# Kernel optimization log

Hardware: AMD Instinct MI355X
Metric: run time of the kernel (lower is better)

The kernel has to match this reference:

```python
import jax, jax.numpy as jnp
import numpy as np

K = 3
S = 1
C_IN = 64
C_OUT = 128

def setup_inputs() -> dict:
    key = jax.random.key(0)
    k1, k2, k3 = jax.random.split(key, 3)
    x = jax.random.normal(k1, (16, C_IN, 256, 256), dtype=jnp.float32)
    weight = jax.random.normal(k2, (C_OUT, C_IN, K, K), dtype=jnp.float32)
    bias = jax.random.normal(k3, (C_OUT,), dtype=jnp.float32)
    return {"x": x, "weight": weight, "bias": bias}

def reference(x, weight, bias):
    # SAME-style padding of k//2 on each side, stride S, output h//S x w//S
    pad = K // 2
    out = jax.lax.conv_general_dilated(
        x, weight,
        window_strides=(S, S),
        padding=[(pad, pad), (pad, pad)],
        dimension_numbers=("NCHW", "OIHW", "NCHW"),
    )
    return out + bias[None, :, None, None]
```

## Files before the change

kernel.cpp:

```cpp
#include <hip/hip_runtime.h>


typedef _Float16 half8_t __attribute__((ext_vector_type(8)));
typedef float floatx4 __attribute__((ext_vector_type(4)));

#define HH 256
#define WW 256
#define CIN 64
#define COUT 128
#define NB 16

#define XP_RSTRIDE   16512
#define XP_NSTRIDE   4260096
#define XP_RSTRIDE_B 33024
#define ROW_LDS      8448
#define TILE_BYTES   50688

__device__ inline void gload_lds16(const void* g, void* l) {
    __builtin_amdgcn_global_load_lds(
        (const __attribute__((address_space(1))) unsigned int*)g,
        (__attribute__((address_space(3))) unsigned int*)l, 16, 0, 0);
}

__global__ void Conv2d_wprep_kernel(const float* __restrict__ w, _Float16* __restrict__ w_t) {
    int idx = blockIdx.x * 256 + threadIdx.x;
    if (idx >= 9 * 8 * 128 * 8) return;
    const int j = idx & 7, cout = (idx >> 3) & 127, s = (idx >> 10) & 7, t = idx >> 13;
    w_t[idx] = (_Float16)w[(cout * 64 + s * 8 + j) * 9 + t];
}

__global__ void Conv2d_xpad_zero_kernel(_Float16* __restrict__ xp) {
    const int idx = blockIdx.x * 256 + threadIdx.x;
    const int n = blockIdx.y;
    if (idx >= 8224) return;
    size_t off;
    if (idx < 2064)      off = (size_t)idx * 8;
    else if (idx < 4128) off = (size_t)257 * XP_RSTRIDE + (size_t)(idx - 2064) * 8;
    else if (idx < 6176) { const int t = idx - 4128;
        off = (size_t)(1 + (t >> 3)) * XP_RSTRIDE + (size_t)(t & 7) * 8; }
    else { const int t = idx - 6176;
        off = (size_t)(1 + (t >> 3)) * XP_RSTRIDE + 257 * 64 + (size_t)(t & 7) * 8; }
    int4 z = {0, 0, 0, 0};
    *(int4*)(xp + (size_t)n * XP_NSTRIDE + off) = z;
}

__global__ __launch_bounds__(256) void Conv2d_xprep_kernel(const float* __restrict__ x,
                                                           _Float16* __restrict__ xp) {
    const int tid = threadIdx.x;
    const int u = tid & 7, colq = tid >> 3;
    const int n = blockIdx.z, h = blockIdx.y;
    const int col0 = blockIdx.x * 128 + colq * 4;

    float4 in[8];
#pragma unroll
    for (int j = 0; j < 8; ++j)
        in[j] = *(const float4*)(x + ((size_t)((n * 64 + u * 8 + j) * 256 + h) * 256) + col0);

    _Float16* dst = xp + (size_t)n * XP_NSTRIDE + (size_t)(h + 1) * XP_RSTRIDE +
                    (size_t)(col0 + 1) * 64 + u * 8;
#pragma unroll
    for (int i = 0; i < 4; ++i) {
        half8_t hv;
#pragma unroll
        for (int j = 0; j < 8; ++j) hv[j] = (_Float16)((const float*)&in[j])[i];
        *(half8_t*)(dst + (size_t)i * 64) = hv;
    }
}

__global__ __launch_bounds__(512, 2) void Conv2dManual_77695958385099_kernel(
    const _Float16* __restrict__ xp, const _Float16* __restrict__ w_t,
    const float* __restrict__ bias, float* __restrict__ out) {
    __shared__ __align__(16) unsigned char xs[2 * TILE_BYTES];
    __shared__ __align__(16) float esc[8][1088];
    const int tid = threadIdx.x;
    const int l = tid & 63, wvid = tid >> 6;
    const int g = l >> 4, ln = l & 15;
    const int ow0 = blockIdx.x * 64;
    const int band = blockIdx.y;
    const int n = blockIdx.z;

    const char* wl = (const char*)w_t + g * 2048 + (wvid * 16 + ln) * 16;
    half8_t A[2][9];
#pragma unroll
    for (int h = 0; h < 2; ++h)
#pragma unroll
        for (int tp = 0; tp < 9; ++tp)
            A[h][tp] = *(const half8_t*)(wl + h * 8192 + tp * 16384);

    const float bv = bias[wvid * 16 + ln];

    int F[4][3][2];
#pragma unroll
    for (int cgf = 0; cgf < 4; ++cgf)
#pragma unroll
        for (int kx = 0; kx < 3; ++kx)
#pragma unroll
            for (int h = 0; h < 2; ++h) {
                const int c = cgf * 16 + kx + ln;
                F[cgf][kx][h] = c * 128 + (((4 * h + g) ^ (c & 7)) << 4);
            }

    const char* xbase = (const char*)xp + (size_t)n * XP_NSTRIDE * 2 + (size_t)ow0 * 128;

#define STAGE(BUFSEL, IT)                                                              \
    {                                                                                  \
        const char* gt = xbase + (size_t)(band * 64 + (IT) * 4) * XP_RSTRIDE_B;        \
        const unsigned lb = (BUFSEL) * TILE_BYTES;                                     \
        _Pragma("unroll")                                                              \
        for (int p = 0; p < 6; ++p) {                                                  \
            const int u = p * 512 + tid;                                               \
            int row = (p * 512) / 528;                                                 \
            if (u >= (row + 1) * 528) row++;                                           \
            const int rem = u - row * 528;                                             \
            const int c = rem >> 3, s = rem & 7;                                       \
            gload_lds16(gt + (size_t)row * XP_RSTRIDE_B + c * 128 +                    \
                            (((s ^ (c & 7))) << 4),                                    \
                        xs + lb + ((unsigned)(p * 512 + (tid & ~63)) << 4));           \
        }                                                                              \
        if (tid < 96) {                                                                \
            const int rem = 432 + tid;                                                 \
            const int c = rem >> 3, s = rem & 7;                                       \
            const int4 v = *(const int4*)(gt + (size_t)5 * XP_RSTRIDE_B + c * 128 +    \
                                          ((s ^ (c & 7)) << 4));                       \
            *(int4*)(xs + lb + (unsigned)(3072 + tid) * 16) = v;                       \
        }                                                                              \
    }

    STAGE(0, 0);
    asm volatile("s_waitcnt vmcnt(0) lgkmcnt(0)" ::: "memory");
    __builtin_amdgcn_s_barrier();
    __builtin_amdgcn_sched_barrier(0);

    int cur = 0;
#pragma unroll 1
    for (int it = 0; it < 16; ++it) {
        if (it < 15) STAGE(cur ^ 1, it + 1);

        floatx4 acc[4][4];
#pragma unroll
        for (int rr = 0; rr < 4; ++rr)
#pragma unroll
            for (int cgf = 0; cgf < 4; ++cgf) acc[rr][cgf] = (floatx4){bv, bv, bv, bv};

        const unsigned char* bb = xs + cur * TILE_BYTES;
#pragma unroll
        for (int kx = 0; kx < 3; ++kx)
#pragma unroll
            for (int h = 0; h < 2; ++h)
#pragma unroll
                for (int cgf = 0; cgf < 4; ++cgf) {
                    const unsigned char* bp = bb + F[cgf][kx][h];
                    half8_t bt[6];
#pragma unroll
                    for (int t = 0; t < 6; ++t)
                        bt[t] = *(const half8_t*)(bp + t * ROW_LDS);
#pragma unroll
                    for (int ky = 0; ky < 3; ++ky) {
                        const half8_t af = A[h][ky * 3 + kx];
#pragma unroll
                        for (int rr = 0; rr < 4; ++rr)
                            acc[rr][cgf] = __builtin_amdgcn_mfma_f32_16x16x32_f16(
                                bt[rr + ky], af, acc[rr][cgf], 0, 0, 0);
                    }
                }

        float* scr = &esc[wvid][0];
        const int orow0 = band * 64 + it * 4;
        float* obase = out + ((size_t)(n * 128 + wvid * 16)) * 65536 +
                       (size_t)orow0 * 256 + ow0;
#pragma unroll
        for (int rr = 0; rr < 4; ++rr) {
#pragma unroll
            for (int cgf = 0; cgf < 4; ++cgf)
                *(floatx4*)(scr + ln * 68 + cgf * 16 + g * 4) = acc[rr][cgf];
#pragma unroll
            for (int q = 0; q < 4; ++q) {
                const int co = q * 4 + g;
                const floatx4 v = *(const floatx4*)(scr + co * 68 + ln * 4);
                __builtin_nontemporal_store(
                    v, (floatx4*)(obase + (size_t)co * 65536 + rr * 256 + ln * 4));
            }
        }

        if (it < 15) {
            asm volatile("s_waitcnt vmcnt(16) lgkmcnt(0)" ::: "memory");
            __builtin_amdgcn_s_barrier();
            __builtin_amdgcn_sched_barrier(0);
        }
        cur ^= 1;
    }
#undef STAGE
}

__global__ __launch_bounds__(256) void Conv2d_fallback_kernel(
    const float* __restrict__ x, const float* __restrict__ w,
    const float* __restrict__ bias, float* __restrict__ out) {
    const int tx = threadIdx.x & 15, ty = threadIdx.x >> 4;
    const int ow0 = blockIdx.x * 64 + tx * 4;
    const int oh = blockIdx.y * 16 + ty;
    const int gg = blockIdx.z & 7, n = blockIdx.z >> 3;
    const int co = gg * 16;
    float acc[16][4];
#pragma unroll
    for (int c = 0; c < 16; ++c) {
        const float b = bias[co + c];
#pragma unroll
        for (int p = 0; p < 4; ++p) acc[c][p] = b;
    }
    const float* xn = x + (size_t)n * CIN * HH * WW;
    const float* wb = w + (size_t)co * CIN * 9;
    for (int ci = 0; ci < CIN; ++ci) {
        const float* xc = xn + (size_t)ci * HH * WW;
        float in[3][6];
#pragma unroll
        for (int ky = 0; ky < 3; ++ky) {
            const int iy = oh + ky - 1;
            if ((unsigned)iy < (unsigned)HH) {
                const float* row = xc + iy * WW;
                const float4 v = *(const float4*)(row + ow0);
                in[ky][1] = v.x; in[ky][2] = v.y; in[ky][3] = v.z; in[ky][4] = v.w;
                in[ky][0] = (ow0 > 0) ? row[ow0 - 1] : 0.0f;
                in[ky][5] = (ow0 < WW - 4) ? row[ow0 + 4] : 0.0f;
            } else {
#pragma unroll
                for (int j = 0; j < 6; ++j) in[ky][j] = 0.0f;
            }
        }
        const float* wc2 = wb + ci * 9;
#pragma unroll
        for (int c = 0; c < 16; ++c) {
            const float* wcc = wc2 + (size_t)c * CIN * 9;
#pragma unroll
            for (int ky = 0; ky < 3; ++ky)
#pragma unroll
                for (int kx = 0; kx < 3; ++kx) {
                    const float wv2 = wcc[ky * 3 + kx];
#pragma unroll
                    for (int p = 0; p < 4; ++p) acc[c][p] += in[ky][kx + p] * wv2;
                }
        }
    }
    const size_t hw = (size_t)HH * WW;
    float* ob = out + ((size_t)n * COUT + co) * hw + (size_t)oh * WW + ow0;
#pragma unroll
    for (int c = 0; c < 16; ++c) {
        float4 v;
        v.x = acc[c][0]; v.y = acc[c][1]; v.z = acc[c][2]; v.w = acc[c][3];
        *(float4*)(ob + (size_t)c * hw) = v;
    }
}

extern "C" void kernel_launch(void* const* d_in, const int* in_sizes, int n_in,
                              void* d_out, int out_size, void* d_ws, size_t ws_size,
                              hipStream_t stream) {
    const float* x = (const float*)d_in[0];
    const float* w = (const float*)d_in[1];
    const float* b = (const float*)d_in[2];
    float* out = (float*)d_out;

    const size_t xp_bytes = (size_t)NB * XP_NSTRIDE * 2;
    const size_t wt_bytes = (size_t)9 * 8 * 128 * 8 * 2;

    if (ws_size >= xp_bytes + wt_bytes) {
        char* ws = (char*)d_ws;
        _Float16* xp = (_Float16*)ws;
        _Float16* w_t = (_Float16*)(ws + xp_bytes);
        Conv2d_wprep_kernel<<<dim3(288), 256, 0, stream>>>(w, w_t);
        Conv2d_xpad_zero_kernel<<<dim3(33, 16), 256, 0, stream>>>(xp);
        Conv2d_xprep_kernel<<<dim3(2, 256, 16), 256, 0, stream>>>(x, xp);
        Conv2dManual_77695958385099_kernel<<<dim3(4, 4, 16), 512, 0, stream>>>(
            xp, w_t, b, out);
    } else {
        dim3 grid(WW / 64, HH / 16, NB * (COUT / 16));
        Conv2d_fallback_kernel<<<grid, 256, 0, stream>>>(x, w, b, out);
    }
}
```

Before: 763.2 us.

## Shrink conv tiles and use a rolling ring buffer of input rows

The main conv kernel moves from 512-thread blocks covering 64 columns × 128 channels to 256-thread blocks covering 32 columns × 64 output channels. The grid grows from 256 to 1024 blocks, which should fill the CUs better. The LDS double buffer of whole 6-row tiles becomes a 10-slot ring of input rows. Each iteration loads only the 4 new rows instead of reloading the overlapping halo rows, which cuts LDS footprint and redundant global loads. The cost is that splitting output channels across blocks reads each input twice, and the smaller per-wave MFMA work lowers reuse of the B operands.

```diff
diff --git a/kernel.cpp b/kernel.cpp
--- a/kernel.cpp
+++ b/kernel.cpp
@@ -13,8 +13,8 @@
 #define XP_RSTRIDE   16512
 #define XP_NSTRIDE   4260096
 #define XP_RSTRIDE_B 33024
-#define ROW_LDS      8448
-#define TILE_BYTES   50688
+#define ROW_LDS      4352
+#define NSLOT        10
 
 __device__ inline void gload_lds16(const void* g, void* l) {
     __builtin_amdgcn_global_load_lds(
@@ -67,19 +67,21 @@
     }
 }
 
-__global__ __launch_bounds__(512, 2) void Conv2dManual_77695958385099_kernel(
+__global__ __launch_bounds__(256, 3) void Conv2dManual_77695958385099_kernel(
     const _Float16* __restrict__ xp, const _Float16* __restrict__ w_t,
     const float* __restrict__ bias, float* __restrict__ out) {
-    __shared__ __align__(16) unsigned char xs[2 * TILE_BYTES];
-    __shared__ __align__(16) float esc[8][1088];
+    __shared__ __align__(16) unsigned char xs[NSLOT * ROW_LDS];
+    __shared__ __align__(16) float esc[4][576];
     const int tid = threadIdx.x;
     const int l = tid & 63, wvid = tid >> 6;
     const int g = l >> 4, ln = l & 15;
-    const int ow0 = blockIdx.x * 64;
+    const int strip = blockIdx.x;
     const int band = blockIdx.y;
-    const int n = blockIdx.z;
-
-    const char* wl = (const char*)w_t + g * 2048 + (wvid * 16 + ln) * 16;
+    const int ch = blockIdx.z & 1, n = blockIdx.z >> 1;
+    const int ow0 = strip * 32;
+    const int co0 = ch * 64;
+
+    const char* wl = (const char*)w_t + g * 2048 + (co0 + wvid * 16 + ln) * 16;
     half8_t A[2][9];
 #pragma unroll
     for (int h = 0; h < 2; ++h)
@@ -87,11 +89,11 @@
         for (int tp = 0; tp < 9; ++tp)
             A[h][tp] = *(const half8_t*)(wl + h * 8192 + tp * 16384);
 
-    const float bv = bias[wvid * 16 + ln];
-
-    int F[4][3][2];
-#pragma unroll
-    for (int cgf = 0; cgf < 4; ++cgf)
+    const float bv = bias[co0 + wvid * 16 + ln];
+
+    int F[2][3][2];
+#pragma unroll
+    for (int cgf = 0; cgf < 2; ++cgf)
 #pragma unroll
         for (int kx = 0; kx < 3; ++kx)
 #pragma unroll
@@ -101,59 +103,78 @@
             }
 
     const char* xbase = (const char*)xp + (size_t)n * XP_NSTRIDE * 2 + (size_t)ow0 * 128;
-
-#define STAGE(BUFSEL, IT)                                                              \
-    {                                                                                  \
-        const char* gt = xbase + (size_t)(band * 64 + (IT) * 4) * XP_RSTRIDE_B;        \
-        const unsigned lb = (BUFSEL) * TILE_BYTES;                                     \
-        _Pragma("unroll")                                                              \
-        for (int p = 0; p < 6; ++p) {                                                  \
-            const int u = p * 512 + tid;                                               \
-            int row = (p * 512) / 528;                                                 \
-            if (u >= (row + 1) * 528) row++;                                           \
-            const int rem = u - row * 528;                                             \
-            const int c = rem >> 3, s = rem & 7;                                       \
-            gload_lds16(gt + (size_t)row * XP_RSTRIDE_B + c * 128 +                    \
-                            (((s ^ (c & 7))) << 4),                                    \
-                        xs + lb + ((unsigned)(p * 512 + (tid & ~63)) << 4));           \
-        }                                                                              \
-        if (tid < 96) {                                                                \
-            const int rem = 432 + tid;                                                 \
-            const int c = rem >> 3, s = rem & 7;                                       \
-            const int4 v = *(const int4*)(gt + (size_t)5 * XP_RSTRIDE_B + c * 128 +    \
-                                          ((s ^ (c & 7)) << 4));                       \
-            *(int4*)(xs + lb + (unsigned)(3072 + tid) * 16) = v;                       \
-        }                                                                              \
-    }
-
-    STAGE(0, 0);
+    const int P0 = band * 64;
+
+#pragma unroll 1
+    for (int j = 0; j < 6; ++j) {
+        const int pr = P0 + j;
+        const int slot = pr % NSLOT;
+        const char* gr = xbase + (size_t)pr * XP_RSTRIDE_B;
+        {
+            const int c = tid >> 3, s = tid & 7;
+            gload_lds16(gr + c * 128 + ((s ^ (c & 7)) << 4),
+                        xs + slot * ROW_LDS + ((tid & ~63) << 4));
+        }
+        if ((tid >> 6) == (j & 3) && (tid & 63) < 16) {
+            const int k = tid & 15;
+            const int c = 32 + (k >> 3), s = k & 7;
+            gload_lds16(gr + c * 128 + ((s ^ (c & 7)) << 4),
+                        xs + slot * ROW_LDS + 4096);
+        }
+    }
     asm volatile("s_waitcnt vmcnt(0) lgkmcnt(0)" ::: "memory");
     __builtin_amdgcn_s_barrier();
     __builtin_amdgcn_sched_barrier(0);
 
-    int cur = 0;
+    int s0 = P0 % NSLOT;
 #pragma unroll 1
     for (int it = 0; it < 16; ++it) {
-        if (it < 15) STAGE(cur ^ 1, it + 1);
-
-        floatx4 acc[4][4];
+        if (it < 15) {
+            const int prn0 = P0 + it * 4 + 6;
+#pragma unroll
+            for (int j = 0; j < 4; ++j) {
+                const int pr = prn0 + j;
+                const int slot = pr % NSLOT;
+                const char* gr = xbase + (size_t)pr * XP_RSTRIDE_B;
+                {
+                    const int c = tid >> 3, s = tid & 7;
+                    gload_lds16(gr + c * 128 + ((s ^ (c & 7)) << 4),
+                                xs + slot * ROW_LDS + ((tid & ~63) << 4));
+                }
+                if ((tid >> 6) == j && (tid & 63) < 16) {
+                    const int k = tid & 15;
+                    const int c = 32 + (k >> 3), s = k & 7;
+                    gload_lds16(gr + c * 128 + ((s ^ (c & 7)) << 4),
+                                xs + slot * ROW_LDS + 4096);
+                }
+            }
+        }
+
+        int roff[6];
+#pragma unroll
+        for (int t = 0; t < 6; ++t) {
+            int st = s0 + t;
+            if (st >= NSLOT) st -= NSLOT;
+            roff[t] = st * ROW_LDS;
+        }
+
+        floatx4 acc[4][2];
 #pragma unroll
         for (int rr = 0; rr < 4; ++rr)
 #pragma unroll
-            for (int cgf = 0; cgf < 4; ++cgf) acc[rr][cgf] = (floatx4){bv, bv, bv, bv};
-
-        const unsigned char* bb = xs + cur * TILE_BYTES;
+            for (int cgf = 0; cgf < 2; ++cgf) acc[rr][cgf] = (floatx4){bv, bv, bv, bv};
+
 #pragma unroll
         for (int kx = 0; kx < 3; ++kx)
 #pragma unroll
             for (int h = 0; h < 2; ++h)
 #pragma unroll
-                for (int cgf = 0; cgf < 4; ++cgf) {
-                    const unsigned char* bp = bb + F[cgf][kx][h];
+                for (int cgf = 0; cgf < 2; ++cgf) {
+                    const unsigned char* bp = xs + F[cgf][kx][h];
                     half8_t bt[6];
 #pragma unroll
                     for (int t = 0; t < 6; ++t)
-                        bt[t] = *(const half8_t*)(bp + t * ROW_LDS);
+                        bt[t] = *(const half8_t*)(bp + roff[t]);
 #pragma unroll
                     for (int ky = 0; ky < 3; ++ky) {
                         const half8_t af = A[h][ky * 3 + kx];
@@ -165,31 +186,30 @@
                 }
 
         float* scr = &esc[wvid][0];
-        const int orow0 = band * 64 + it * 4;
-        float* obase = out + ((size_t)(n * 128 + wvid * 16)) * 65536 +
-                       (size_t)orow0 * 256 + ow0;
+        float* obase = out + ((size_t)(n * 128 + co0 + wvid * 16)) * 65536 +
+                       (size_t)(P0 + it * 4) * 256 + ow0;
 #pragma unroll
         for (int rr = 0; rr < 4; ++rr) {
 #pragma unroll
-            for (int cgf = 0; cgf < 4; ++cgf)
-                *(floatx4*)(scr + ln * 68 + cgf * 16 + g * 4) = acc[rr][cgf];
-#pragma unroll
-            for (int q = 0; q < 4; ++q) {
-                const int co = q * 4 + g;
-                const floatx4 v = *(const floatx4*)(scr + co * 68 + ln * 4);
+            for (int cgf = 0; cgf < 2; ++cgf)
+                *(floatx4*)(scr + ln * 36 + cgf * 16 + g * 4) = acc[rr][cgf];
+#pragma unroll
+            for (int q = 0; q < 2; ++q) {
+                const int co = q * 8 + g * 2 + (ln >> 3);
+                const floatx4 v = *(const floatx4*)(scr + co * 36 + (ln & 7) * 4);
                 __builtin_nontemporal_store(
-                    v, (floatx4*)(obase + (size_t)co * 65536 + rr * 256 + ln * 4));
+                    v, (floatx4*)(obase + (size_t)co * 65536 + rr * 256 + (ln & 7) * 4));
             }
         }
 
         if (it < 15) {
-            asm volatile("s_waitcnt vmcnt(16) lgkmcnt(0)" ::: "memory");
+            asm volatile("s_waitcnt vmcnt(8) lgkmcnt(0)" ::: "memory");
             __builtin_amdgcn_s_barrier();
             __builtin_amdgcn_sched_barrier(0);
         }
-        cur ^= 1;
-    }
-#undef STAGE
+        s0 += 4;
+        if (s0 >= NSLOT) s0 -= NSLOT;
+    }
 }
 
 __global__ __launch_bounds__(256) void Conv2d_fallback_kernel(
@@ -268,7 +288,7 @@
         Conv2d_wprep_kernel<<<dim3(288), 256, 0, stream>>>(w, w_t);
         Conv2d_xpad_zero_kernel<<<dim3(33, 16), 256, 0, stream>>>(xp);
         Conv2d_xprep_kernel<<<dim3(2, 256, 16), 256, 0, stream>>>(x, xp);
-        Conv2dManual_77695958385099_kernel<<<dim3(4, 4, 16), 512, 0, stream>>>(
+        Conv2dManual_77695958385099_kernel<<<dim3(8, 4, 32), 256, 0, stream>>>(
             xp, w_t, b, out);
     } else {
         dim3 grid(WW / 64, HH / 16, NB * (COUT / 16));
```

Result: slower. 779.2 us (+2.1%).

## Fuse input fp16 conversion and padding into conv kernel with row ring buffer

Applied to the files above, without the earlier changes.

Removes the separate pad-zero and NCHW-to-padded-NHWC fp16 prep kernels. The main conv kernel now reads fp32 input directly, converts it to fp16 in registers and writes swizzled rows into a 10-slot LDS ring, so each iteration loads only 4 new rows instead of a 6-row double-buffered tile. This drops a full write and re-read of the fp16 intermediate and the extra launches. In exchange, global loads are register-staged instead of going direct to LDS, halo columns are gathered with scalar loads, and conversion ALU work is added inside the compute loop.

```diff
diff --git a/kernel.cpp b/kernel.cpp
--- a/kernel.cpp
+++ b/kernel.cpp
@@ -10,17 +10,8 @@
 #define COUT 128
 #define NB 16
 
-#define XP_RSTRIDE   16512
-#define XP_NSTRIDE   4260096
-#define XP_RSTRIDE_B 33024
-#define ROW_LDS      8448
-#define TILE_BYTES   50688
-
-__device__ inline void gload_lds16(const void* g, void* l) {
-    __builtin_amdgcn_global_load_lds(
-        (const __attribute__((address_space(1))) unsigned int*)g,
-        (__attribute__((address_space(3))) unsigned int*)l, 16, 0, 0);
-}
+#define ROW_LDS 8448
+#define NSLOT   10
 
 __global__ void Conv2d_wprep_kernel(const float* __restrict__ w, _Float16* __restrict__ w_t) {
     int idx = blockIdx.x * 256 + threadIdx.x;
@@ -29,48 +20,10 @@
     w_t[idx] = (_Float16)w[(cout * 64 + s * 8 + j) * 9 + t];
 }
 
-__global__ void Conv2d_xpad_zero_kernel(_Float16* __restrict__ xp) {
-    const int idx = blockIdx.x * 256 + threadIdx.x;
-    const int n = blockIdx.y;
-    if (idx >= 8224) return;
-    size_t off;
-    if (idx < 2064)      off = (size_t)idx * 8;
-    else if (idx < 4128) off = (size_t)257 * XP_RSTRIDE + (size_t)(idx - 2064) * 8;
-    else if (idx < 6176) { const int t = idx - 4128;
-        off = (size_t)(1 + (t >> 3)) * XP_RSTRIDE + (size_t)(t & 7) * 8; }
-    else { const int t = idx - 6176;
-        off = (size_t)(1 + (t >> 3)) * XP_RSTRIDE + 257 * 64 + (size_t)(t & 7) * 8; }
-    int4 z = {0, 0, 0, 0};
-    *(int4*)(xp + (size_t)n * XP_NSTRIDE + off) = z;
-}
-
-__global__ __launch_bounds__(256) void Conv2d_xprep_kernel(const float* __restrict__ x,
-                                                           _Float16* __restrict__ xp) {
-    const int tid = threadIdx.x;
-    const int u = tid & 7, colq = tid >> 3;
-    const int n = blockIdx.z, h = blockIdx.y;
-    const int col0 = blockIdx.x * 128 + colq * 4;
-
-    float4 in[8];
-#pragma unroll
-    for (int j = 0; j < 8; ++j)
-        in[j] = *(const float4*)(x + ((size_t)((n * 64 + u * 8 + j) * 256 + h) * 256) + col0);
-
-    _Float16* dst = xp + (size_t)n * XP_NSTRIDE + (size_t)(h + 1) * XP_RSTRIDE +
-                    (size_t)(col0 + 1) * 64 + u * 8;
-#pragma unroll
-    for (int i = 0; i < 4; ++i) {
-        half8_t hv;
-#pragma unroll
-        for (int j = 0; j < 8; ++j) hv[j] = (_Float16)((const float*)&in[j])[i];
-        *(half8_t*)(dst + (size_t)i * 64) = hv;
-    }
-}
-
 __global__ __launch_bounds__(512, 2) void Conv2dManual_77695958385099_kernel(
-    const _Float16* __restrict__ xp, const _Float16* __restrict__ w_t,
+    const float* __restrict__ x, const _Float16* __restrict__ w_t,
     const float* __restrict__ bias, float* __restrict__ out) {
-    __shared__ __align__(16) unsigned char xs[2 * TILE_BYTES];
+    __shared__ __align__(16) unsigned char xs[NSLOT * ROW_LDS];
     __shared__ __align__(16) float esc[8][1088];
     const int tid = threadIdx.x;
     const int l = tid & 63, wvid = tid >> 6;
@@ -78,6 +31,14 @@
     const int ow0 = blockIdx.x * 64;
     const int band = blockIdx.y;
     const int n = blockIdx.z;
+    const int P0 = band * 64;
+
+    const int rw = tid >> 7;
+    const int t7 = tid & 127;
+    const int su = t7 & 7;
+    const int cb = t7 >> 3;
+    const bool isEdge = (t7 >= 120);
+    const int eu = t7 - 120;
 
     const char* wl = (const char*)w_t + g * 2048 + (wvid * 16 + ln) * 16;
     half8_t A[2][9];
@@ -100,41 +61,79 @@
                 F[cgf][kx][h] = c * 128 + (((4 * h + g) ^ (c & 7)) << 4);
             }
 
-    const char* xbase = (const char*)xp + (size_t)n * XP_NSTRIDE * 2 + (size_t)ow0 * 128;
-
-#define STAGE(BUFSEL, IT)                                                              \
-    {                                                                                  \
-        const char* gt = xbase + (size_t)(band * 64 + (IT) * 4) * XP_RSTRIDE_B;        \
-        const unsigned lb = (BUFSEL) * TILE_BYTES;                                     \
-        _Pragma("unroll")                                                              \
-        for (int p = 0; p < 6; ++p) {                                                  \
-            const int u = p * 512 + tid;                                               \
-            int row = (p * 512) / 528;                                                 \
-            if (u >= (row + 1) * 528) row++;                                           \
-            const int rem = u - row * 528;                                             \
-            const int c = rem >> 3, s = rem & 7;                                       \
-            gload_lds16(gt + (size_t)row * XP_RSTRIDE_B + c * 128 +                    \
-                            (((s ^ (c & 7))) << 4),                                    \
-                        xs + lb + ((unsigned)(p * 512 + (tid & ~63)) << 4));           \
-        }                                                                              \
-        if (tid < 96) {                                                                \
-            const int rem = 432 + tid;                                                 \
-            const int c = rem >> 3, s = rem & 7;                                       \
-            const int4 v = *(const int4*)(gt + (size_t)5 * XP_RSTRIDE_B + c * 128 +    \
-                                          ((s ^ (c & 7)) << 4));                       \
-            *(int4*)(xs + lb + (unsigned)(3072 + tid) * 16) = v;                       \
-        }                                                                              \
-    }
-
-    STAGE(0, 0);
-    asm volatile("s_waitcnt vmcnt(0) lgkmcnt(0)" ::: "memory");
+    auto stage_load = [&](int pr, float4 (&ld)[8], float (&e0)[8], float (&e1)[8]) {
+        const int gr = pr - 1;
+        const bool vrow = ((unsigned)gr < 256u);
+        if (vrow) {
+            const float4* xr = (const float4*)x +
+                               (((size_t)(n * 64 + su * 8)) << 14) +
+                               (size_t)gr * 64 + (ow0 >> 2) + cb;
+#pragma unroll
+            for (int j = 0; j < 8; ++j) ld[j] = xr[(size_t)j << 14];
+        } else {
+#pragma unroll
+            for (int j = 0; j < 8; ++j) ld[j] = (float4){0.f, 0.f, 0.f, 0.f};
+        }
+        if (isEdge) {
+            const float* xe = x + (((size_t)(n * 64 + eu * 8)) << 16) + (size_t)gr * 256;
+#pragma unroll
+            for (int j = 0; j < 8; ++j) {
+                e0[j] = (vrow && ow0 > 0)        ? xe[((size_t)j << 16) + ow0 - 1]  : 0.f;
+                e1[j] = (vrow && ow0 + 64 < 256) ? xe[((size_t)j << 16) + ow0 + 64] : 0.f;
+            }
+        }
+    };
+    auto stage_write = [&](int pr, const float4 (&ld)[8], const float (&e0)[8],
+                           const float (&e1)[8]) {
+        const unsigned sb = (unsigned)(pr % NSLOT) * ROW_LDS;
+#pragma unroll
+        for (int k = 0; k < 4; ++k) {
+            const int c = 1 + cb * 4 + k;
+            half8_t hv;
+#pragma unroll
+            for (int j = 0; j < 8; ++j) hv[j] = (_Float16)((const float*)&ld[j])[k];
+            *(half8_t*)(xs + sb + c * 128 + ((su ^ (c & 7)) << 4)) = hv;
+        }
+        if (isEdge) {
+            half8_t h0, h1;
+#pragma unroll
+            for (int j = 0; j < 8; ++j) {
+                h0[j] = (_Float16)e0[j];
+                h1[j] = (_Float16)e1[j];
+            }
+            *(half8_t*)(xs + sb + (eu << 4)) = h0;
+            *(half8_t*)(xs + sb + 65 * 128 + ((eu ^ 1) << 4)) = h1;
+        }
+    };
+
+    {
+        float4 ld[8]; float e0[8], e1[8];
+        stage_load(P0 + rw, ld, e0, e1);
+        stage_write(P0 + rw, ld, e0, e1);
+        if (rw < 2) {
+            stage_load(P0 + 4 + rw, ld, e0, e1);
+            stage_write(P0 + 4 + rw, ld, e0, e1);
+        }
+    }
+    asm volatile("s_waitcnt lgkmcnt(0)" ::: "memory");
     __builtin_amdgcn_s_barrier();
     __builtin_amdgcn_sched_barrier(0);
 
-    int cur = 0;
+    int s0 = P0 % NSLOT;
 #pragma unroll 1
     for (int it = 0; it < 16; ++it) {
-        if (it < 15) STAGE(cur ^ 1, it + 1);
+        float4 ld[8]; float e0[8], e1[8];
+        const int prn = P0 + it * 4 + 6 + rw;
+        if (it < 15) stage_load(prn, ld, e0, e1);
+        __builtin_amdgcn_sched_barrier(0);
+
+        int roff[6];
+#pragma unroll
+        for (int tt = 0; tt < 6; ++tt) {
+            int st = s0 + tt;
+            if (st >= NSLOT) st -= NSLOT;
+            roff[tt] = st * ROW_LDS;
+        }
 
         floatx4 acc[4][4];
 #pragma unroll
@@ -142,18 +141,17 @@
 #pragma unroll
             for (int cgf = 0; cgf < 4; ++cgf) acc[rr][cgf] = (floatx4){bv, bv, bv, bv};
 
-        const unsigned char* bb = xs + cur * TILE_BYTES;
 #pragma unroll
         for (int kx = 0; kx < 3; ++kx)
 #pragma unroll
             for (int h = 0; h < 2; ++h)
 #pragma unroll
                 for (int cgf = 0; cgf < 4; ++cgf) {
-                    const unsigned char* bp = bb + F[cgf][kx][h];
+                    const unsigned char* bp = xs + F[cgf][kx][h];
                     half8_t bt[6];
 #pragma unroll
-                    for (int t = 0; t < 6; ++t)
-                        bt[t] = *(const half8_t*)(bp + t * ROW_LDS);
+                    for (int tt = 0; tt < 6; ++tt)
+                        bt[tt] = *(const half8_t*)(bp + roff[tt]);
 #pragma unroll
                     for (int ky = 0; ky < 3; ++ky) {
                         const half8_t af = A[h][ky * 3 + kx];
@@ -165,9 +163,8 @@
                 }
 
         float* scr = &esc[wvid][0];
-        const int orow0 = band * 64 + it * 4;
         float* obase = out + ((size_t)(n * 128 + wvid * 16)) * 65536 +
-                       (size_t)orow0 * 256 + ow0;
+                       (size_t)(P0 + it * 4) * 256 + ow0;
 #pragma unroll
         for (int rr = 0; rr < 4; ++rr) {
 #pragma unroll
@@ -183,13 +180,14 @@
         }
 
         if (it < 15) {
-            asm volatile("s_waitcnt vmcnt(16) lgkmcnt(0)" ::: "memory");
+            stage_write(prn, ld, e0, e1);
+            asm volatile("s_waitcnt lgkmcnt(0)" ::: "memory");
             __builtin_amdgcn_s_barrier();
             __builtin_amdgcn_sched_barrier(0);
         }
-        cur ^= 1;
-    }
-#undef STAGE
+        s0 += 4;
+        if (s0 >= NSLOT) s0 -= NSLOT;
+    }
 }
 
 __global__ __launch_bounds__(256) void Conv2d_fallback_kernel(
@@ -258,18 +256,13 @@
     const float* b = (const float*)d_in[2];
     float* out = (float*)d_out;
 
-    const size_t xp_bytes = (size_t)NB * XP_NSTRIDE * 2;
     const size_t wt_bytes = (size_t)9 * 8 * 128 * 8 * 2;
 
-    if (ws_size >= xp_bytes + wt_bytes) {
-        char* ws = (char*)d_ws;
-        _Float16* xp = (_Float16*)ws;
-        _Float16* w_t = (_Float16*)(ws + xp_bytes);
+    if (ws_size >= wt_bytes) {
+        _Float16* w_t = (_Float16*)d_ws;
         Conv2d_wprep_kernel<<<dim3(288), 256, 0, stream>>>(w, w_t);
-        Conv2d_xpad_zero_kernel<<<dim3(33, 16), 256, 0, stream>>>(xp);
-        Conv2d_xprep_kernel<<<dim3(2, 256, 16), 256, 0, stream>>>(x, xp);
         Conv2dManual_77695958385099_kernel<<<dim3(4, 4, 16), 512, 0, stream>>>(
-            xp, w_t, b, out);
+            x, w_t, b, out);
     } else {
         dim3 grid(WW / 64, HH / 16, NB * (COUT / 16));
         Conv2d_fallback_kernel<<<grid, 256, 0, stream>>>(x, w, b, out);
```

Result: no change. 749.8 us (-1.8%).
